# Performance work log

Hardware: AMD Instinct MI355X
Metric: run time of the kernel (lower is better)

Reference implementation:

```python
import jax, jax.numpy as jnp
import numpy as np

EPS = 1e-5  # BatchNorm2d default eps

def setup_inputs() -> dict:
    key = jax.random.key(0)
    k1, k2, k3, k4 = jax.random.split(key, 4)
    B, Cin, Cout, T, V = 64, 64, 128, 300, 25
    x = jax.random.normal(k1, (B, Cin, T, V), dtype=jnp.float32)
    adj = jax.random.uniform(k2, (V, V), dtype=jnp.float32)
    # Conv2d(kernel_size=1) weight (Cout, Cin), kaiming-ish scale
    W = jax.random.normal(k3, (Cout, Cin), dtype=jnp.float32) * (1.0 / np.sqrt(Cin))
    b = jnp.zeros((Cout,), dtype=jnp.float32)
    gamma = jnp.ones((Cout,), dtype=jnp.float32)
    beta = jnp.zeros((Cout,), dtype=jnp.float32)
    return {"x": x, "adj": adj, "W": W, "b": b, "gamma": gamma, "beta": beta}

def reference(x, adj, W, b, gamma, beta):
    # x: (B, C, T, V); graph aggregation over joints: matmul with adj on last dim
    xg = jnp.einsum('bctv,vw->bctw', x, adj)
    # 1x1 conv == per-(t,v) channel projection
    y = jnp.einsum('bctv,oc->botv', xg, W) + b[None, :, None, None]
    # BatchNorm2d (training mode): per-channel stats over (B, T, V), biased var
    mean = jnp.mean(y, axis=(0, 2, 3), keepdims=True)
    var = jnp.mean((y - mean) ** 2, axis=(0, 2, 3), keepdims=True)
    yn = (y - mean) * jax.lax.rsqrt(var + EPS)
    out = jax.nn.relu(gamma[None, :, None, None] * yn + beta[None, :, None, None])
    return out
```

## Files before the change

kernel.cpp:

```cpp
#include <hip/hip_runtime.h>
#include <stdint.h>

typedef __attribute__((ext_vector_type(8)))  short   short8;
typedef __attribute__((ext_vector_type(4)))  short   short4v;
typedef __attribute__((ext_vector_type(16))) float   floatx16;

#define B_    64
#define CIN   64
#define COUT  128
#define T_    300
#define V_    25
#define TV    (T_ * V_)
#define NRED  (B_ * T_ * V_)
#define NSLOTS 32
#define EPS   1e-5f


__device__ __forceinline__ unsigned short f2bf(float f) {
    union { float f; uint32_t u; } c; c.f = f;
    uint32_t u = c.u;
    u += 0x7FFFu + ((u >> 16) & 1u);
    return (unsigned short)(u >> 16);
}

__device__ __forceinline__ floatx16 fzero16() {
    floatx16 z;
#pragma unroll
    for (int i = 0; i < 16; ++i) z[i] = 0.f;
    return z;
}

__global__ void pack_kernel(const float* __restrict__ W, const float* __restrict__ adj,
                            unsigned short* __restrict__ wsW, unsigned short* __restrict__ wsAdj) {
    int stride = blockDim.x * gridDim.x;
    for (int idx = threadIdx.x + blockIdx.x * blockDim.x; idx < 8192; idx += stride) {
        int j  = idx & 7;
        int l  = (idx >> 3) & 63;
        int kk = (idx >> 9) & 3;
        int w  = idx >> 11;
        int o  = 32 * w + (l & 31);
        int c  = 16 * kk + 8 * (l >> 5) + j;
        wsW[idx] = f2bf(W[o * CIN + c]);
    }
    for (int idx = threadIdx.x + blockIdx.x * blockDim.x; idx < 1024; idx += stride) {
        int j = idx & 7;
        int l = (idx >> 3) & 63;
        int s = idx >> 9;
        int k = 16 * s + 8 * (l >> 5) + j;
        int n = l & 31;
        float v = (k < V_ && n < V_) ? adj[k * V_ + n] : 0.f;
        wsAdj[idx] = f2bf(v);
    }
}

template <bool WRITE>
__global__ __launch_bounds__(256) void main_kernel(
    const float* __restrict__ x,
    const unsigned short* __restrict__ wsW,
    const unsigned short* __restrict__ wsAdj,
    const float* __restrict__ scale, const float* __restrict__ shift,
    float* __restrict__ psum, float* __restrict__ psq,
    float* __restrict__ out)
{
    __shared__ unsigned short Gbuf[2][2048] __attribute__((aligned(16)));

    const int tid  = threadIdx.x;
    const int wave = tid >> 6;
    const int lane = tid & 63;
    const int q    = lane >> 5;
    const int ln   = lane & 31;
    const int b    = blockIdx.y;
    const int t0   = blockIdx.x * 4;
    const int ctile = wave & 1;
    const int tsel  = wave >> 1;

    short8 wf[4];
#pragma unroll
    for (int kk = 0; kk < 4; ++kk)
        wf[kk] = ((const short8*)wsW)[(wave * 4 + kk) * 64 + lane];
    short8 af[2];
#pragma unroll
    for (int s = 0; s < 2; ++s)
        af[s] = ((const short8*)wsAdj)[s * 64 + lane];

    float sc[16], sh[16], sums[16], sqs[16];
    if (WRITE) {
#pragma unroll
        for (int r = 0; r < 16; ++r) {
            int row = 32 * wave + (r & 3) + 8 * (r >> 2) + 4 * q;
            sc[r] = scale[row];
            sh[r] = shift[row];
        }
    } else {
#pragma unroll
        for (int r = 0; r < 16; ++r) { sums[r] = 0.f; sqs[r] = 0.f; }
    }

    for (int iter = 0; iter < 2; ++iter) {
        const int t = t0 + iter * 2 + tsel;
        const float* xrow = x + ((size_t)(b * CIN + 32 * ctile + ln) * T_ + t) * V_;

        short8 xa0, xa1;
#pragma unroll
        for (int j = 0; j < 8; ++j) xa0[j] = (short)f2bf(xrow[8 * q + j]);
        if (q == 0) {
#pragma unroll
            for (int j = 0; j < 8; ++j) xa1[j] = (short)f2bf(xrow[16 + j]);
        } else {
            xa1[0] = (short)f2bf(xrow[24]);
#pragma unroll
            for (int j = 1; j < 8; ++j) xa1[j] = 0;
        }

        floatx16 g = fzero16();
        g = __builtin_amdgcn_mfma_f32_32x32x16_bf16(xa0, af[0], g, 0, 0, 0);
        g = __builtin_amdgcn_mfma_f32_32x32x16_bf16(xa1, af[1], g, 0, 0, 0);

        __syncthreads();

#pragma unroll
        for (int r1 = 0; r1 < 4; ++r1) {
            short4v p;
#pragma unroll
            for (int r0 = 0; r0 < 4; ++r0) p[r0] = (short)f2bf(g[r1 * 4 + r0]);
            *(short4v*)&Gbuf[tsel][((4 * ctile + r1) * 32 + ln) * 8 + 4 * q] = p;
        }

        __syncthreads();

#pragma unroll
        for (int ts = 0; ts < 2; ++ts) {
            floatx16 acc = fzero16();
#pragma unroll
            for (int kk = 0; kk < 4; ++kk) {
                short8 bfrag = *(const short8*)&Gbuf[ts][((kk * 2 + q) * 32 + ln) * 8];
                acc = __builtin_amdgcn_mfma_f32_32x32x16_bf16(wf[kk], bfrag, acc, 0, 0, 0);
            }
            if (WRITE) {
                const int t_out = t0 + iter * 2 + ts;
                if (ln < V_) {
                    float* obase = out + ((size_t)(b * COUT + 32 * wave) * T_ + t_out) * V_ + ln;
#pragma unroll
                    for (int r = 0; r < 16; ++r) {
                        int row = (r & 3) + 8 * (r >> 2) + 4 * q;
                        float v = sc[r] * acc[r] + sh[r];
                        obase[(size_t)row * TV] = v > 0.f ? v : 0.f;
                    }
                }
            } else {
#pragma unroll
                for (int r = 0; r < 16; ++r) {
                    sums[r] += acc[r];
                    sqs[r]  += acc[r] * acc[r];
                }
            }
        }
    }

    if (!WRITE) {
#pragma unroll
        for (int r = 0; r < 16; ++r) {
            float s = sums[r], ss = sqs[r];
#pragma unroll
            for (int m = 1; m <= 16; m <<= 1) {
                s  += __shfl_xor(s,  m, 64);
                ss += __shfl_xor(ss, m, 64);
            }
            sums[r] = s; sqs[r] = ss;
        }
        if (ln == 0) {
            int slot = (blockIdx.y * 75 + blockIdx.x) & (NSLOTS - 1);
#pragma unroll
            for (int r = 0; r < 16; ++r) {
                int ch = 32 * wave + (r & 3) + 8 * (r >> 2) + 4 * q;
                atomicAdd(&psum[slot * COUT + ch], sums[r]);
                atomicAdd(&psq [slot * COUT + ch], sqs[r]);
            }
        }
    }
}

__global__ void stats_kernel(const float* __restrict__ psum, const float* __restrict__ psq,
                             const float* __restrict__ gamma, const float* __restrict__ beta,
                             float* __restrict__ scale, float* __restrict__ shift) {
    int o = threadIdx.x;
    float s = 0.f, ss = 0.f;
    for (int k = 0; k < NSLOTS; ++k) {
        s  += psum[k * COUT + o];
        ss += psq [k * COUT + o];
    }
    float mean = s / (float)NRED;
    float var  = ss / (float)NRED - mean * mean;
    float inv  = rsqrtf(var + EPS);
    float scv  = gamma[o] * inv;
    scale[o] = scv;
    shift[o] = beta[o] - mean * scv;
}

extern "C" void kernel_launch(void* const* d_in, const int* in_sizes, int n_in,
                              void* d_out, int out_size, void* d_ws, size_t ws_size,
                              hipStream_t stream) {
    const float* x     = (const float*)d_in[0];
    const float* adj   = (const float*)d_in[1];
    const float* W     = (const float*)d_in[2];
    const float* gamma = (const float*)d_in[4];
    const float* beta  = (const float*)d_in[5];
    float* out = (float*)d_out;

    char* ws = (char*)d_ws;
    unsigned short* wsW   = (unsigned short*)(ws);
    unsigned short* wsAdj = (unsigned short*)(ws + 16384);
    float* psum  = (float*)(ws + 18432);
    float* psq   = (float*)(ws + 34816);
    float* scale = (float*)(ws + 51200);
    float* shift = (float*)(ws + 51712);

    hipMemsetAsync(psum, 0, 2 * NSLOTS * COUT * sizeof(float), stream);

    pack_kernel<<<8, 256, 0, stream>>>(W, adj, wsW, wsAdj);

    dim3 grid(75, 64);
    main_kernel<false><<<grid, 256, 0, stream>>>(x, wsW, wsAdj, nullptr, nullptr, psum, psq, nullptr);
    stats_kernel<<<1, 128, 0, stream>>>(psum, psq, gamma, beta, scale, shift);
    main_kernel<true><<<grid, 256, 0, stream>>>(x, wsW, wsAdj, scale, shift, psum, psq, out);
}
```

Measured before the change: 464.6 us.

## Stash bf16 graph-aggregated fragments between passes and drop LDS exchange

Each wave now computes the adjacency product for all input channels itself and reorders fragments with lane shuffles instead of an LDS buffer and two barriers. Each block processes 12 time steps rather than 4, so there are fewer blocks. When the workspace is large enough, pass 1 writes the bf16 aggregated fragments to global memory, and pass 2 reads them back instead of reloading fp32 x and redoing the first matmul. The packed bf16 intermediate is half the size of x. The cost is redundant adjacency MFMAs across the four waves and an extra write of the intermediate in pass 1.

```diff
diff --git a/kernel.cpp b/kernel.cpp
--- a/kernel.cpp
+++ b/kernel.cpp
@@ -1,8 +1,8 @@
 #include <hip/hip_runtime.h>
+#include <hip/hip_bf16.h>
 #include <stdint.h>
 
 typedef __attribute__((ext_vector_type(8)))  short   short8;
-typedef __attribute__((ext_vector_type(4)))  short   short4v;
 typedef __attribute__((ext_vector_type(16))) float   floatx16;
 
 #define B_    64
@@ -13,8 +13,11 @@
 #define TV    (T_ * V_)
 #define NRED  (B_ * T_ * V_)
 #define NSLOTS 32
+#define NT    12
 #define EPS   1e-5f
 
+#define GFRAG_OFF   65536
+#define GFRAG_BYTES ((size_t)B_ * T_ * 4 * 64 * 8 * 2)
 
 __device__ __forceinline__ unsigned short f2bf(float f) {
     union { float f; uint32_t u; } c; c.f = f;
@@ -23,11 +26,65 @@
     return (unsigned short)(u >> 16);
 }
 
+__device__ __forceinline__ uint32_t pk2(float a, float b) {
+    union { __hip_bfloat162 h; uint32_t u; } c;
+    c.h = __float22bfloat162_rn(make_float2(a, b));
+    return c.u;
+}
+
 __device__ __forceinline__ floatx16 fzero16() {
     floatx16 z;
 #pragma unroll
     for (int i = 0; i < 16; ++i) z[i] = 0.f;
     return z;
+}
+
+__device__ __forceinline__ void build_xfrags(const float* __restrict__ x,
+                                             int b, int t, int ln, int q,
+                                             short8 xa[2][2]) {
+#pragma unroll
+    for (int ct = 0; ct < 2; ++ct) {
+        const float* xr = x + ((size_t)(b * CIN + 32 * ct + ln) * T_ + t) * V_;
+        union { short8 s; uint32_t u[4]; } A0, A1;
+#pragma unroll
+        for (int p = 0; p < 4; ++p)
+            A0.u[p] = pk2(xr[8 * q + 2 * p], xr[8 * q + 2 * p + 1]);
+        if (q == 0) {
+#pragma unroll
+            for (int p = 0; p < 4; ++p)
+                A1.u[p] = pk2(xr[16 + 2 * p], xr[16 + 2 * p + 1]);
+        } else {
+            A1.u[0] = pk2(xr[24], 0.f);
+            A1.u[1] = 0; A1.u[2] = 0; A1.u[3] = 0;
+        }
+        xa[ct][0] = A0.s;
+        xa[ct][1] = A1.s;
+    }
+}
+
+__device__ __forceinline__ void compute_g_frags(const short8 xa[2][2],
+                                                const short8 af[2], int q,
+                                                short8 frag[4]) {
+#pragma unroll
+    for (int ct = 0; ct < 2; ++ct) {
+        floatx16 g = fzero16();
+        g = __builtin_amdgcn_mfma_f32_32x32x16_bf16(xa[ct][0], af[0], g, 0, 0, 0);
+        g = __builtin_amdgcn_mfma_f32_32x32x16_bf16(xa[ct][1], af[1], g, 0, 0, 0);
+        uint32_t pk[8], pp[8];
+#pragma unroll
+        for (int i = 0; i < 8; ++i) pk[i] = pk2(g[2 * i], g[2 * i + 1]);
+#pragma unroll
+        for (int i = 0; i < 8; ++i) pp[i] = (uint32_t)__shfl_xor((int)pk[i], 32, 64);
+#pragma unroll
+        for (int kkl = 0; kkl < 2; ++kkl) {
+            union { short8 s; uint32_t u[4]; } F;
+            F.u[0] = q ? pp[4 * kkl + 2] : pk[4 * kkl];
+            F.u[1] = q ? pp[4 * kkl + 3] : pk[4 * kkl + 1];
+            F.u[2] = q ? pk[4 * kkl + 2] : pp[4 * kkl];
+            F.u[3] = q ? pk[4 * kkl + 3] : pp[4 * kkl + 1];
+            frag[2 * ct + kkl] = F.s;
+        }
+    }
 }
 
 __global__ void pack_kernel(const float* __restrict__ W, const float* __restrict__ adj,
@@ -53,26 +110,21 @@
     }
 }
 
-template <bool WRITE>
-__global__ __launch_bounds__(256) void main_kernel(
+template <bool STASH>
+__global__ __launch_bounds__(256, 3) void pass1_kernel(
     const float* __restrict__ x,
     const unsigned short* __restrict__ wsW,
     const unsigned short* __restrict__ wsAdj,
-    const float* __restrict__ scale, const float* __restrict__ shift,
     float* __restrict__ psum, float* __restrict__ psq,
-    float* __restrict__ out)
+    unsigned short* __restrict__ gfrag)
 {
-    __shared__ unsigned short Gbuf[2][2048] __attribute__((aligned(16)));
-
     const int tid  = threadIdx.x;
     const int wave = tid >> 6;
     const int lane = tid & 63;
     const int q    = lane >> 5;
     const int ln   = lane & 31;
     const int b    = blockIdx.y;
-    const int t0   = blockIdx.x * 4;
-    const int ctile = wave & 1;
-    const int tsel  = wave >> 1;
+    const int tbase = blockIdx.x * NT;
 
     short8 wf[4];
 #pragma unroll
@@ -83,99 +135,51 @@
     for (int s = 0; s < 2; ++s)
         af[s] = ((const short8*)wsAdj)[s * 64 + lane];
 
-    float sc[16], sh[16], sums[16], sqs[16];
-    if (WRITE) {
+    float sums[16], sqs[16];
+#pragma unroll
+    for (int r = 0; r < 16; ++r) { sums[r] = 0.f; sqs[r] = 0.f; }
+
+    for (int i = 0; i < NT; ++i) {
+        const int t = tbase + i;
+        short8 xa[2][2];
+        build_xfrags(x, b, t, ln, q, xa);
+        short8 frag[4];
+        compute_g_frags(xa, af, q, frag);
+
+        if (STASH && wave == 0) {
+            short8* gp = (short8*)gfrag + (size_t)(b * T_ + t) * 4 * 64 + lane;
+#pragma unroll
+            for (int kk = 0; kk < 4; ++kk) gp[kk * 64] = frag[kk];
+        }
+
+        floatx16 acc = fzero16();
+#pragma unroll
+        for (int kk = 0; kk < 4; ++kk)
+            acc = __builtin_amdgcn_mfma_f32_32x32x16_bf16(wf[kk], frag[kk], acc, 0, 0, 0);
 #pragma unroll
         for (int r = 0; r < 16; ++r) {
-            int row = 32 * wave + (r & 3) + 8 * (r >> 2) + 4 * q;
-            sc[r] = scale[row];
-            sh[r] = shift[row];
-        }
-    } else {
-#pragma unroll
-        for (int r = 0; r < 16; ++r) { sums[r] = 0.f; sqs[r] = 0.f; }
-    }
-
-    for (int iter = 0; iter < 2; ++iter) {
-        const int t = t0 + iter * 2 + tsel;
-        const float* xrow = x + ((size_t)(b * CIN + 32 * ctile + ln) * T_ + t) * V_;
-
-        short8 xa0, xa1;
-#pragma unroll
-        for (int j = 0; j < 8; ++j) xa0[j] = (short)f2bf(xrow[8 * q + j]);
-        if (q == 0) {
-#pragma unroll
-            for (int j = 0; j < 8; ++j) xa1[j] = (short)f2bf(xrow[16 + j]);
-        } else {
-            xa1[0] = (short)f2bf(xrow[24]);
-#pragma unroll
-            for (int j = 1; j < 8; ++j) xa1[j] = 0;
-        }
-
-        floatx16 g = fzero16();
-        g = __builtin_amdgcn_mfma_f32_32x32x16_bf16(xa0, af[0], g, 0, 0, 0);
-        g = __builtin_amdgcn_mfma_f32_32x32x16_bf16(xa1, af[1], g, 0, 0, 0);
-
-        __syncthreads();
-
-#pragma unroll
-        for (int r1 = 0; r1 < 4; ++r1) {
-            short4v p;
-#pragma unroll
-            for (int r0 = 0; r0 < 4; ++r0) p[r0] = (short)f2bf(g[r1 * 4 + r0]);
-            *(short4v*)&Gbuf[tsel][((4 * ctile + r1) * 32 + ln) * 8 + 4 * q] = p;
-        }
-
-        __syncthreads();
-
-#pragma unroll
-        for (int ts = 0; ts < 2; ++ts) {
-            floatx16 acc = fzero16();
-#pragma unroll
-            for (int kk = 0; kk < 4; ++kk) {
-                short8 bfrag = *(const short8*)&Gbuf[ts][((kk * 2 + q) * 32 + ln) * 8];
-                acc = __builtin_amdgcn_mfma_f32_32x32x16_bf16(wf[kk], bfrag, acc, 0, 0, 0);
-            }
-            if (WRITE) {
-                const int t_out = t0 + iter * 2 + ts;
-                if (ln < V_) {
-                    float* obase = out + ((size_t)(b * COUT + 32 * wave) * T_ + t_out) * V_ + ln;
-#pragma unroll
-                    for (int r = 0; r < 16; ++r) {
-                        int row = (r & 3) + 8 * (r >> 2) + 4 * q;
-                        float v = sc[r] * acc[r] + sh[r];
-                        obase[(size_t)row * TV] = v > 0.f ? v : 0.f;
-                    }
-                }
-            } else {
-#pragma unroll
-                for (int r = 0; r < 16; ++r) {
-                    sums[r] += acc[r];
-                    sqs[r]  += acc[r] * acc[r];
-                }
-            }
-        }
-    }
-
-    if (!WRITE) {
+            sums[r] += acc[r];
+            sqs[r]  += acc[r] * acc[r];
+        }
+    }
+
+#pragma unroll
+    for (int r = 0; r < 16; ++r) {
+        float s = sums[r], ss = sqs[r];
+#pragma unroll
+        for (int m = 1; m <= 16; m <<= 1) {
+            s  += __shfl_xor(s,  m, 64);
+            ss += __shfl_xor(ss, m, 64);
+        }
+        sums[r] = s; sqs[r] = ss;
+    }
+    if (ln == 0) {
+        int slot = (blockIdx.y * 25 + blockIdx.x) & (NSLOTS - 1);
 #pragma unroll
         for (int r = 0; r < 16; ++r) {
-            float s = sums[r], ss = sqs[r];
-#pragma unroll
-            for (int m = 1; m <= 16; m <<= 1) {
-                s  += __shfl_xor(s,  m, 64);
-                ss += __shfl_xor(ss, m, 64);
-            }
-            sums[r] = s; sqs[r] = ss;
-        }
-        if (ln == 0) {
-            int slot = (blockIdx.y * 75 + blockIdx.x) & (NSLOTS - 1);
-#pragma unroll
-            for (int r = 0; r < 16; ++r) {
-                int ch = 32 * wave + (r & 3) + 8 * (r >> 2) + 4 * q;
-                atomicAdd(&psum[slot * COUT + ch], sums[r]);
-                atomicAdd(&psq [slot * COUT + ch], sqs[r]);
-            }
+            int ch = 32 * wave + (r & 3) + 8 * (r >> 2) + 4 * q;
+            atomicAdd(&psum[slot * COUT + ch], sums[r]);
+            atomicAdd(&psq [slot * COUT + ch], sqs[r]);
         }
     }
 }
@@ -195,6 +199,72 @@
     float scv  = gamma[o] * inv;
     scale[o] = scv;
     shift[o] = beta[o] - mean * scv;
+}
+
+template <bool STASH>
+__global__ __launch_bounds__(256, 3) void pass2_kernel(
+    const float* __restrict__ x,
+    const unsigned short* __restrict__ wsW,
+    const unsigned short* __restrict__ wsAdj,
+    const unsigned short* __restrict__ gfrag,
+    const float* __restrict__ scale, const float* __restrict__ shift,
+    float* __restrict__ out)
+{
+    const int tid  = threadIdx.x;
+    const int wave = tid >> 6;
+    const int lane = tid & 63;
+    const int q    = lane >> 5;
+    const int ln   = lane & 31;
+    const int b    = blockIdx.y;
+    const int tbase = blockIdx.x * NT;
+
+    short8 wf[4];
+#pragma unroll
+    for (int kk = 0; kk < 4; ++kk)
+        wf[kk] = ((const short8*)wsW)[(wave * 4 + kk) * 64 + lane];
+    short8 af[2];
+    if (!STASH) {
+#pragma unroll
+        for (int s = 0; s < 2; ++s)
+            af[s] = ((const short8*)wsAdj)[s * 64 + lane];
+    }
+
+    float sc[16], sh[16];
+#pragma unroll
+    for (int r = 0; r < 16; ++r) {
+        int row = 32 * wave + (r & 3) + 8 * (r >> 2) + 4 * q;
+        sc[r] = scale[row];
+        sh[r] = shift[row];
+    }
+
+    for (int i = 0; i < NT; ++i) {
+        const int t = tbase + i;
+        short8 frag[4];
+        if (STASH) {
+            const short8* gp = (const short8*)gfrag + (size_t)(b * T_ + t) * 4 * 64 + lane;
+#pragma unroll
+            for (int kk = 0; kk < 4; ++kk) frag[kk] = gp[kk * 64];
+        } else {
+            short8 xa[2][2];
+            build_xfrags(x, b, t, ln, q, xa);
+            compute_g_frags(xa, af, q, frag);
+        }
+
+        floatx16 acc = fzero16();
+#pragma unroll
+        for (int kk = 0; kk < 4; ++kk)
+            acc = __builtin_amdgcn_mfma_f32_32x32x16_bf16(wf[kk], frag[kk], acc, 0, 0, 0);
+
+        if (ln < V_) {
+            float* obase = out + ((size_t)(b * COUT + 32 * wave) * T_ + t) * V_ + ln;
+#pragma unroll
+            for (int r = 0; r < 16; ++r) {
+                int row = (r & 3) + 8 * (r >> 2) + 4 * q;
+                float v = sc[r] * acc[r] + sh[r];
+                obase[(size_t)row * TV] = v > 0.f ? v : 0.f;
+            }
+        }
+    }
 }
 
 extern "C" void kernel_launch(void* const* d_in, const int* in_sizes, int n_in,
@@ -214,13 +284,21 @@
     float* psq   = (float*)(ws + 34816);
     float* scale = (float*)(ws + 51200);
     float* shift = (float*)(ws + 51712);
+    unsigned short* gfrag = (unsigned short*)(ws + GFRAG_OFF);
+
+    const bool stash = ws_size >= (size_t)GFRAG_OFF + GFRAG_BYTES;
 
     hipMemsetAsync(psum, 0, 2 * NSLOTS * COUT * sizeof(float), stream);
-
     pack_kernel<<<8, 256, 0, stream>>>(W, adj, wsW, wsAdj);
 
-    dim3 grid(75, 64);
-    main_kernel<false><<<grid, 256, 0, stream>>>(x, wsW, wsAdj, nullptr, nullptr, psum, psq, nullptr);
-    stats_kernel<<<1, 128, 0, stream>>>(psum, psq, gamma, beta, scale, shift);
-    main_kernel<true><<<grid, 256, 0, stream>>>(x, wsW, wsAdj, scale, shift, psum, psq, out);
-}
+    dim3 grid(T_ / NT, B_);
+    if (stash) {
+        pass1_kernel<true><<<grid, 256, 0, stream>>>(x, wsW, wsAdj, psum, psq, gfrag);
+        stats_kernel<<<1, 128, 0, stream>>>(psum, psq, gamma, beta, scale, shift);
+        pass2_kernel<true><<<grid, 256, 0, stream>>>(x, wsW, wsAdj, gfrag, scale, shift, out);
+    } else {
+        pass1_kernel<false><<<grid, 256, 0, stream>>>(x, wsW, wsAdj, psum, psq, gfrag);
+        stats_kernel<<<1, 128, 0, stream>>>(psum, psq, gamma, beta, scale, shift);
+        pass2_kernel<false><<<grid, 256, 0, stream>>>(x, wsW, wsAdj, gfrag, scale, shift, out);
+    }
+}
```

New measurement: 542.6 us. 16.8% more time.
